# Performance work log

Hardware: AMD Instinct MI355X
Metric: run time of the kernel (lower is better)

The kernel has to match this reference:

```python
import jax, jax.numpy as jnp
import numpy as np

N_NODES = 100000
N_EDGES = 1000000
IN_CH = 128
HID = 128
N_CLS = 3


def setup_inputs() -> dict:
    key = jax.random.key(0)
    ks = jax.random.split(key, 10)
    scale_in = 1.0 / np.sqrt(IN_CH)
    scale_h = 1.0 / np.sqrt(HID)
    return {
        "x": jax.random.normal(ks[0], (N_NODES, IN_CH), dtype=jnp.float32),
        "edge_index": jax.random.randint(ks[1], (2, N_EDGES), 0, N_NODES, dtype=jnp.int64),
        # SAGEConv layer 1: lin_l (aggregated neighbors, with bias), lin_r (root, no bias)
        "w_l1": jax.random.normal(ks[2], (IN_CH, HID), dtype=jnp.float32) * scale_in,
        "b_l1": jnp.zeros((HID,), dtype=jnp.float32),
        "w_r1": jax.random.normal(ks[3], (IN_CH, HID), dtype=jnp.float32) * scale_in,
        # SAGEConv layer 2
        "w_l2": jax.random.normal(ks[4], (HID, HID), dtype=jnp.float32) * scale_h,
        "b_l2": jnp.zeros((HID,), dtype=jnp.float32),
        "w_r2": jax.random.normal(ks[5], (HID, HID), dtype=jnp.float32) * scale_h,
        # final classifier
        "w_cls": jax.random.normal(ks[6], (HID, N_CLS), dtype=jnp.float32) * scale_h,
        "b_cls": jnp.zeros((N_CLS,), dtype=jnp.float32),
    }


def _sage_conv(x, src, dst, w_l, b_l, w_r, num_nodes):
    # mean aggregation of source-node features onto destination nodes
    msg = x[src]                                              # [E, C] gather
    agg = jax.ops.segment_sum(msg, dst, num_segments=num_nodes)
    cnt = jax.ops.segment_sum(jnp.ones((src.shape[0],), x.dtype), dst,
                              num_segments=num_nodes)
    mean = agg / jnp.maximum(cnt, 1.0)[:, None]
    # out = lin_l(mean_aggr) + lin_r(x)
    return mean @ w_l + b_l + x @ w_r


def reference(x, edge_index, w_l1, b_l1, w_r1, w_l2, b_l2, w_r2, w_cls, b_cls):
    src, dst = edge_index[0], edge_index[1]
    n = x.shape[0]
    h = jax.nn.relu(_sage_conv(x, src, dst, w_l1, b_l1, w_r1, n))
    # dropout is identity in eval mode
    h = jax.nn.relu(_sage_conv(h, src, dst, w_l2, b_l2, w_r2, n))
    logits = h @ w_cls + b_cls
    return logits
```

## Files before the change

kernel.cpp:

```cpp
#include <hip/hip_runtime.h>
#include <hip/hip_bf16.h>

#define N_NODES 100000
#define N_EDGES 1000000
#define CH 128
#define KTOT 256
#define NCLS 3
#define SCAN_B 1024
#define SCAN_NB ((N_NODES + SCAN_B - 1) / SCAN_B)

#define NB_CNT ((N_EDGES + 255) / 256)
#define NB_CVTX (N_NODES * CH / 4 / 256)
#define NB_CVTW (KTOT * CH / 256)
#define NB_OTHER (NB_CVTX + 2 * NB_CVTW)
#define NB_PRE (NB_CNT + NB_OTHER)

typedef __attribute__((ext_vector_type(8))) short v8s;
typedef __attribute__((ext_vector_type(4))) float v4f;

__device__ __forceinline__ float bf2f(unsigned short u) {
    return __uint_as_float(((unsigned int)u) << 16);
}

__device__ __forceinline__ unsigned short f2bf(float f) {
    unsigned int u = __float_as_uint(f);
    unsigned int r = (u + 0x7fffu + ((u >> 16) & 1u)) >> 16;
    return (unsigned short)r;
}

__device__ __forceinline__ int edge_at(const void* e, int is64, long long i) {
    if (is64) return (int)((const long long*)e)[i];
    return ((const int*)e)[i];
}

__device__ __forceinline__ float ldf(const void* p, int isbf, size_t i) {
    if (isbf) return bf2f(((const unsigned short*)p)[i]);
    return ((const float*)p)[i];
}

__device__ __forceinline__ void acc_u32(unsigned int u, float& a0, float& a1) {
    a0 += bf2f((unsigned short)(u & 0xffffu));
    a1 += bf2f((unsigned short)(u >> 16));
}

__global__ void k_init(const void* __restrict__ e, const unsigned int* __restrict__ x,
                       int* __restrict__ eflag, int* __restrict__ dtf,
                       int* __restrict__ cnt, int* __restrict__ done) {
    int b = blockIdx.x;
    if (b == 0) {
        if (threadIdx.x < 64) {
            int v = ((const int*)e)[2 * threadIdx.x + 1];
            unsigned long long bl = __ballot(v != 0);
            if (threadIdx.x == 0) *eflag = (bl == 0ULL) ? 1 : 0;
        } else if (threadIdx.x == 64) {
            *done = 0;
        }
    } else if (b == 1) {
        if (threadIdx.x < 64) {
            unsigned int u = x[threadIdx.x];
            int ex = (u >> 7) & 0xff;
            int sane = (ex == 0) || (ex >= 100 && ex <= 154);
            unsigned long long bl = __ballot(sane);
            if (threadIdx.x == 0) *dtf = (__popcll(bl) >= 48) ? 1 : 0;
        }
    } else {
        int i = (b - 2) * 256 + threadIdx.x;
        if (i < N_NODES) cnt[i] = 0;
    }
}

__global__ void k_pre(const void* __restrict__ e, const int* __restrict__ eflag,
                      const int* __restrict__ dtf,
                      int* __restrict__ cnt, unsigned short* __restrict__ epos,
                      const void* __restrict__ x, unsigned short* __restrict__ Abuf,
                      const void* __restrict__ wl1, const void* __restrict__ wr1,
                      unsigned short* __restrict__ WT1,
                      const void* __restrict__ wl2, const void* __restrict__ wr2,
                      unsigned short* __restrict__ WT2) {
    int b = blockIdx.x;
    int cb = (b + 3) >> 2;
    if (cb > NB_CNT) cb = NB_CNT;
    if ((b & 3) == 0 && (b >> 2) < NB_CNT) {
        int i = (b >> 2) * 256 + threadIdx.x;
        if (i >= N_EDGES) return;
        int is64 = *eflag;
        int dst = edge_at(e, is64, (long long)N_EDGES + i);
        epos[i] = (unsigned short)atomicAdd(&cnt[dst], 1);
    } else {
        int ob = b - cb;
        if (ob < NB_CVTX) {
            int idx = ob * 256 + threadIdx.x;
            int node = idx >> 5;
            int ch = (idx & 31) * 4;
            int isbf = *dtf;
            unsigned short o[4];
            if (isbf) {
                ushort4 u = *(const ushort4*)((const unsigned short*)x +
                                              (size_t)node * CH + ch);
                o[0] = u.x; o[1] = u.y; o[2] = u.z; o[3] = u.w;
            } else {
                float4 v = *(const float4*)((const float*)x + (size_t)node * CH + ch);
                o[0] = f2bf(v.x); o[1] = f2bf(v.y); o[2] = f2bf(v.z); o[3] = f2bf(v.w);
            }
            *(ushort4*)(Abuf + (size_t)node * KTOT + CH + ch) =
                make_ushort4(o[0], o[1], o[2], o[3]);
        } else {
            int rel = ob - NB_CVTX;
            const void* wl = (rel < NB_CVTW) ? wl1 : wl2;
            const void* wr = (rel < NB_CVTW) ? wr1 : wr2;
            unsigned short* WT = (rel < NB_CVTW) ? WT1 : WT2;
            int i = (rel % NB_CVTW) * 256 + threadIdx.x;
            int k = i >> 7;
            int n = i & 127;
            int isbf = *dtf;
            float v = (k < CH) ? ldf(wl, isbf, (size_t)k * CH + n)
                               : ldf(wr, isbf, (size_t)(k - CH) * CH + n);
            WT[(size_t)n * KTOT + k] = f2bf(v);
        }
    }
}

__global__ __launch_bounds__(SCAN_B) void k_scan(
    const int* __restrict__ cnt, int* __restrict__ bsum, int* __restrict__ done,
    int* __restrict__ row_start) {
    __shared__ int s[SCAN_B];
    __shared__ int spre_sh;
    int tid = threadIdx.x;
    int gid = blockIdx.x * SCAN_B + tid;
    int v = (gid < N_NODES) ? cnt[gid] : 0;
    s[tid] = v;
    __syncthreads();
    for (int off = 1; off < SCAN_B; off <<= 1) {
        int t = (tid >= off) ? s[tid - off] : 0;
        __syncthreads();
        s[tid] += t;
        __syncthreads();
    }
    int excl_val = s[tid] - v;
    if (tid == SCAN_B - 1) {
        bsum[blockIdx.x] = s[tid];
        __threadfence();
        atomicAdd(done, 1);
    }
    if (tid == 0) {
        while (__hip_atomic_load(done, __ATOMIC_ACQUIRE, __HIP_MEMORY_SCOPE_AGENT) <
               SCAN_NB) {
        }
        __threadfence();
        int run = 0;
        for (int r = 0; r < SCAN_NB; r++) {
            if (r >= (int)blockIdx.x) break;
            run += bsum[r];
        }
        spre_sh = run;
    }
    __syncthreads();
    if (gid < N_NODES) row_start[gid] = excl_val + spre_sh;
    if (gid == 0) row_start[N_NODES] = N_EDGES;
}

__global__ void k_bucket(const void* __restrict__ e, const int* __restrict__ eflag,
                         const int* __restrict__ row_start,
                         const unsigned short* __restrict__ epos,
                         int* __restrict__ csr_src) {
    int i = blockIdx.x * blockDim.x + threadIdx.x;
    if (i >= N_EDGES) return;
    int is64 = *eflag;
    int src = edge_at(e, is64, i);
    int dst = edge_at(e, is64, (long long)N_EDGES + i);
    csr_src[row_start[dst] + (int)epos[i]] = src;
}

__global__ __launch_bounds__(256) void k_agg(
    const int* __restrict__ row_start, const int* __restrict__ csr_src,
    const unsigned short* __restrict__ gsrc, unsigned short* __restrict__ gdst) {
    long long gt = (long long)blockIdx.x * blockDim.x + threadIdx.x;
    int node = (int)(gt >> 4);
    int lane = (int)(gt & 15);
    if (node >= N_NODES) return;
    int beg = row_start[node];
    int end = row_start[node + 1];
    float a[8];
#pragma unroll
    for (int j = 0; j < 8; j++) a[j] = 0.f;
    int e = beg;
    while (e + 8 <= end) {
        int s[8];
#pragma unroll
        for (int j = 0; j < 8; j++) s[j] = csr_src[e + j];
        uint4 u[8];
#pragma unroll
        for (int j = 0; j < 8; j++)
            u[j] = *(const uint4*)(gsrc + (size_t)s[j] * KTOT + CH + lane * 8);
#pragma unroll
        for (int j = 0; j < 8; j++) {
            acc_u32(u[j].x, a[0], a[1]); acc_u32(u[j].y, a[2], a[3]);
            acc_u32(u[j].z, a[4], a[5]); acc_u32(u[j].w, a[6], a[7]);
        }
        e += 8;
    }
    while (e + 2 <= end) {
        int s0 = csr_src[e], s1 = csr_src[e + 1];
        uint4 u0 = *(const uint4*)(gsrc + (size_t)s0 * KTOT + CH + lane * 8);
        uint4 u1 = *(const uint4*)(gsrc + (size_t)s1 * KTOT + CH + lane * 8);
        acc_u32(u0.x, a[0], a[1]); acc_u32(u0.y, a[2], a[3]);
        acc_u32(u0.z, a[4], a[5]); acc_u32(u0.w, a[6], a[7]);
        acc_u32(u1.x, a[0], a[1]); acc_u32(u1.y, a[2], a[3]);
        acc_u32(u1.z, a[4], a[5]); acc_u32(u1.w, a[6], a[7]);
        e += 2;
    }
    if (e < end) {
        int s0 = csr_src[e];
        uint4 u0 = *(const uint4*)(gsrc + (size_t)s0 * KTOT + CH + lane * 8);
        acc_u32(u0.x, a[0], a[1]); acc_u32(u0.y, a[2], a[3]);
        acc_u32(u0.z, a[4], a[5]); acc_u32(u0.w, a[6], a[7]);
    }
    float rinv = 1.0f / (float)max(end - beg, 1);
    unsigned int p0 = (unsigned int)f2bf(a[0] * rinv) | ((unsigned int)f2bf(a[1] * rinv) << 16);
    unsigned int p1 = (unsigned int)f2bf(a[2] * rinv) | ((unsigned int)f2bf(a[3] * rinv) << 16);
    unsigned int p2 = (unsigned int)f2bf(a[4] * rinv) | ((unsigned int)f2bf(a[5] * rinv) << 16);
    unsigned int p3 = (unsigned int)f2bf(a[6] * rinv) | ((unsigned int)f2bf(a[7] * rinv) << 16);
    *(uint4*)(gdst + (size_t)node * KTOT + lane * 8) = make_uint4(p0, p1, p2, p3);
}

#define LDK 40
#define CLS_LD 130
__global__ __launch_bounds__(256) void k_gemm_mfma(
    const unsigned short* __restrict__ Abuf, const unsigned short* __restrict__ WT,
    const void* __restrict__ bias, const int* __restrict__ dtf,
    unsigned short* __restrict__ out, int out_stride, int out_off,
    const void* __restrict__ wcls, const void* __restrict__ bcls,
    float* __restrict__ cls_out) {
    __shared__ unsigned short smem[4 * 128 * LDK];
    __shared__ float wcls_s[CH * NCLS];
    unsigned short* As = smem;
    unsigned short* Bs = smem + 2 * 128 * LDK;
    const int t = threadIdx.x;
    const int w = t >> 6, l = t & 63;
    const int wx = w & 1, wy = w >> 1;
    const int quad = l >> 4, lrow = l & 15;
    const int row0 = blockIdx.x * 128;
    const int srow = t >> 1, shalf = t & 1;
    const int isbf = *dtf;

    if (cls_out) {
        for (int i = t; i < CH * NCLS; i += 256) wcls_s[i] = ldf(wcls, isbf, i);
    }

    int ar = row0 + srow;
    if (ar >= N_NODES) ar = N_NODES - 1;
    const unsigned short* abase = Abuf + (size_t)ar * KTOT + shalf * 16;
    const unsigned short* bbase = WT + (size_t)srow * KTOT + shalf * 16;

    v4f acc[4][4];
#pragma unroll
    for (int i = 0; i < 4; i++)
#pragma unroll
        for (int j = 0; j < 4; j++) acc[i][j] = (v4f){0.f, 0.f, 0.f, 0.f};

    {
        uint4 a0 = *(const uint4*)abase, a1 = *(const uint4*)(abase + 8);
        uint4 b0 = *(const uint4*)bbase, b1 = *(const uint4*)(bbase + 8);
        *(uint4*)&As[srow * LDK + shalf * 16] = a0;
        *(uint4*)&As[srow * LDK + shalf * 16 + 8] = a1;
        *(uint4*)&Bs[srow * LDK + shalf * 16] = b0;
        *(uint4*)&Bs[srow * LDK + shalf * 16 + 8] = b1;
    }
#pragma unroll
    for (int k = 0; k < KTOT / 32; k++) {
        uint4 na0, na1, nb0, nb1;
        if (k < KTOT / 32 - 1) {
            na0 = *(const uint4*)(abase + (k + 1) * 32);
            na1 = *(const uint4*)(abase + (k + 1) * 32 + 8);
            nb0 = *(const uint4*)(bbase + (k + 1) * 32);
            nb1 = *(const uint4*)(bbase + (k + 1) * 32 + 8);
        }
        __syncthreads();
        const int cur = (k & 1) * 128 * LDK, nxt = ((k + 1) & 1) * 128 * LDK;
        v8s af[4], bfr[4];
#pragma unroll
        for (int mi = 0; mi < 4; mi++)
            af[mi] = *(const v8s*)&As[cur + (wy * 64 + mi * 16 + lrow) * LDK + quad * 8];
#pragma unroll
        for (int ni = 0; ni < 4; ni++)
            bfr[ni] = *(const v8s*)&Bs[cur + (wx * 64 + ni * 16 + lrow) * LDK + quad * 8];
#pragma unroll
        for (int mi = 0; mi < 4; mi++)
#pragma unroll
            for (int ni = 0; ni < 4; ni++)
                acc[mi][ni] = __builtin_amdgcn_mfma_f32_16x16x32_bf16(
                    af[mi], bfr[ni], acc[mi][ni], 0, 0, 0);
        if (k < KTOT / 32 - 1) {
            *(uint4*)&As[nxt + srow * LDK + shalf * 16] = na0;
            *(uint4*)&As[nxt + srow * LDK + shalf * 16 + 8] = na1;
            *(uint4*)&Bs[nxt + srow * LDK + shalf * 16] = nb0;
            *(uint4*)&Bs[nxt + srow * LDK + shalf * 16 + 8] = nb1;
        }
    }
    float bj[4];
#pragma unroll
    for (int ni = 0; ni < 4; ni++) bj[ni] = ldf(bias, isbf, wx * 64 + ni * 16 + lrow);

    if (!cls_out) {
#pragma unroll
        for (int mi = 0; mi < 4; mi++) {
#pragma unroll
            for (int r = 0; r < 4; r++) {
                int grow = row0 + wy * 64 + mi * 16 + quad * 4 + r;
                if (grow < N_NODES) {
#pragma unroll
                    for (int ni = 0; ni < 4; ni++) {
                        int col = wx * 64 + ni * 16 + lrow;
                        float v = fmaxf(acc[mi][ni][r] + bj[ni], 0.0f);
                        out[(size_t)grow * out_stride + out_off + col] = f2bf(v);
                    }
                }
            }
        }
    } else {
        __syncthreads();
#pragma unroll
        for (int mi = 0; mi < 4; mi++) {
#pragma unroll
            for (int r = 0; r < 4; r++) {
                int row = wy * 64 + mi * 16 + quad * 4 + r;
#pragma unroll
                for (int ni = 0; ni < 4; ni++) {
                    int col = wx * 64 + ni * 16 + lrow;
                    float v = fmaxf(acc[mi][ni][r] + bj[ni], 0.0f);
                    smem[row * CLS_LD + col] = f2bf(v);
                }
            }
        }
        __syncthreads();
        if (t < 128) {
            int grow = row0 + t;
            if (grow < N_NODES) {
                float a0 = 0.f, a1 = 0.f, a2 = 0.f;
                for (int k = 0; k < CH; k++) {
                    float h = bf2f(smem[t * CLS_LD + k]);
                    a0 += h * wcls_s[k * NCLS + 0];
                    a1 += h * wcls_s[k * NCLS + 1];
                    a2 += h * wcls_s[k * NCLS + 2];
                }
                cls_out[(size_t)grow * NCLS + 0] = a0 + ldf(bcls, isbf, 0);
                cls_out[(size_t)grow * NCLS + 1] = a1 + ldf(bcls, isbf, 1);
                cls_out[(size_t)grow * NCLS + 2] = a2 + ldf(bcls, isbf, 2);
            }
        }
    }
}

extern "C" void kernel_launch(void* const* d_in, const int* in_sizes, int n_in,
                              void* d_out, int out_size, void* d_ws, size_t ws_size,
                              hipStream_t stream) {
    const void* x = d_in[0];
    const void* eidx = d_in[1];
    const void* w_l1 = d_in[2];
    const void* b_l1 = d_in[3];
    const void* w_r1 = d_in[4];
    const void* w_l2 = d_in[5];
    const void* b_l2 = d_in[6];
    const void* w_r2 = d_in[7];
    const void* w_cls = d_in[8];
    const void* b_cls = d_in[9];

    char* w = (char*)d_ws;
    int* eflag = (int*)w;
    int* dtf = (int*)(w + 64);
    int* done = (int*)(w + 128);
    int* cnt = (int*)(w + 4096);
    int* row_start = (int*)(w + 405504);
    int* bsum = (int*)(w + 1207296);
    unsigned short* epos = (unsigned short*)(w + 2097152);
    int* csr_src = (int*)(w + 4194304);
    unsigned short* WT1 = (unsigned short*)(w + 8388608);
    unsigned short* WT2 = (unsigned short*)(w + 8454144);
    unsigned short* A1 = (unsigned short*)(w + 11534336);
    unsigned short* A2 = (unsigned short*)(w + 62914560);

    hipLaunchKernelGGL(k_init, dim3(2 + (N_NODES + 255) / 256), dim3(256), 0, stream,
                       eidx, (const unsigned int*)x, eflag, dtf, cnt, done);
    hipLaunchKernelGGL(k_pre, dim3(NB_PRE), dim3(256), 0, stream,
                       eidx, eflag, dtf, cnt, epos, x, A1,
                       w_l1, w_r1, WT1, w_l2, w_r2, WT2);
    hipLaunchKernelGGL(k_scan, dim3(SCAN_NB), dim3(SCAN_B), 0, stream,
                       cnt, bsum, done, row_start);
    hipLaunchKernelGGL(k_bucket, dim3(NB_CNT), dim3(256), 0, stream,
                       eidx, eflag, row_start, epos, csr_src);
    hipLaunchKernelGGL(k_agg, dim3(N_NODES * 16 / 256), dim3(256), 0, stream,
                       row_start, csr_src, A1, A1);
    hipLaunchKernelGGL(k_gemm_mfma, dim3((N_NODES + 127) / 128), dim3(256), 0, stream,
                       A1, WT1, b_l1, dtf, A2, KTOT, CH,
                       (const void*)nullptr, (const void*)nullptr, (float*)nullptr);
    hipLaunchKernelGGL(k_agg, dim3(N_NODES * 16 / 256), dim3(256), 0, stream,
                       row_start, csr_src, A2, A2);
    hipLaunchKernelGGL(k_gemm_mfma, dim3((N_NODES + 127) / 128), dim3(256), 0, stream,
                       A2, WT2, b_l2, dtf, (unsigned short*)nullptr, 0, 0,
                       w_cls, b_cls, (float*)d_out);
}
```

Baseline: 302.2 us.

## Privatize degree counters per XCD and fuse scan with edge bucketing

Degree counting now keeps a separate counter array for each XCD, selected by reading the hardware XCD id register, so the atomics from one XCD no longer contend with the other seven across dies. Each edge stores its XCD index in the top bits of its 16-bit rank. The scan kernel sums the eight per-XCD counts, writes per-XCD base offsets back into the counter arrays, then waits on a grid-wide barrier before all 488 blocks scatter edges into CSR. This removes one kernel launch and the cross-die atomic traffic, at the cost of eight times the counter memory to zero and read, and a spin barrier that needs all blocks to be resident at once. The rank field is limited to 12 bits.

```diff
diff --git a/kernel.cpp b/kernel.cpp
--- a/kernel.cpp
+++ b/kernel.cpp
@@ -8,12 +8,12 @@
 #define NCLS 3
 #define SCAN_B 1024
 #define SCAN_NB ((N_NODES + SCAN_B - 1) / SCAN_B)
+#define SB_BLOCKS 488
 
 #define NB_CNT ((N_EDGES + 255) / 256)
 #define NB_CVTX (N_NODES * CH / 4 / 256)
 #define NB_CVTW (KTOT * CH / 256)
-#define NB_OTHER (NB_CVTX + 2 * NB_CVTW)
-#define NB_PRE (NB_CNT + NB_OTHER)
+#define NB_PRE (NB_CNT + NB_CVTX + 2 * NB_CVTW)
 
 typedef __attribute__((ext_vector_type(8))) short v8s;
 typedef __attribute__((ext_vector_type(4))) float v4f;
@@ -43,9 +43,13 @@
     a1 += bf2f((unsigned short)(u >> 16));
 }
 
+__device__ __forceinline__ int xcd_id() {
+    return (int)(__builtin_amdgcn_s_getreg(6164) & 7u);
+}
+
 __global__ void k_init(const void* __restrict__ e, const unsigned int* __restrict__ x,
                        int* __restrict__ eflag, int* __restrict__ dtf,
-                       int* __restrict__ cnt, int* __restrict__ done) {
+                       int* __restrict__ cnt8, int* __restrict__ done) {
     int b = blockIdx.x;
     if (b == 0) {
         if (threadIdx.x < 64) {
@@ -53,7 +57,8 @@
             unsigned long long bl = __ballot(v != 0);
             if (threadIdx.x == 0) *eflag = (bl == 0ULL) ? 1 : 0;
         } else if (threadIdx.x == 64) {
-            *done = 0;
+            done[0] = 0;
+            done[1] = 0;
         }
     } else if (b == 1) {
         if (threadIdx.x < 64) {
@@ -65,13 +70,13 @@
         }
     } else {
         int i = (b - 2) * 256 + threadIdx.x;
-        if (i < N_NODES) cnt[i] = 0;
+        if (i < 8 * N_NODES) cnt8[i] = 0;
     }
 }
 
 __global__ void k_pre(const void* __restrict__ e, const int* __restrict__ eflag,
                       const int* __restrict__ dtf,
-                      int* __restrict__ cnt, unsigned short* __restrict__ epos,
+                      int* __restrict__ cnt8, unsigned short* __restrict__ epos,
                       const void* __restrict__ x, unsigned short* __restrict__ Abuf,
                       const void* __restrict__ wl1, const void* __restrict__ wr1,
                       unsigned short* __restrict__ WT1,
@@ -85,7 +90,9 @@
         if (i >= N_EDGES) return;
         int is64 = *eflag;
         int dst = edge_at(e, is64, (long long)N_EDGES + i);
-        epos[i] = (unsigned short)atomicAdd(&cnt[dst], 1);
+        int r = xcd_id();
+        int rank = atomicAdd(&cnt8[r * N_NODES + dst], 1);
+        epos[i] = (unsigned short)(rank | (r << 12));
     } else {
         int ob = b - cb;
         if (ob < NB_CVTX) {
@@ -120,55 +127,78 @@
     }
 }
 
-__global__ __launch_bounds__(SCAN_B) void k_scan(
-    const int* __restrict__ cnt, int* __restrict__ bsum, int* __restrict__ done,
-    int* __restrict__ row_start) {
-    __shared__ int s[SCAN_B];
-    __shared__ int spre_sh;
-    int tid = threadIdx.x;
-    int gid = blockIdx.x * SCAN_B + tid;
-    int v = (gid < N_NODES) ? cnt[gid] : 0;
-    s[tid] = v;
+__global__ __launch_bounds__(SCAN_B) void k_scan_bucket(
+    int* __restrict__ cnt8, int* __restrict__ bsum, int* __restrict__ done,
+    int* __restrict__ row_start, const void* __restrict__ e,
+    const int* __restrict__ eflag, const unsigned short* __restrict__ epos,
+    int* __restrict__ csr_src) {
+    int tid = threadIdx.x, bid = blockIdx.x;
+    if (bid < SCAN_NB) {
+        __shared__ int s[SCAN_B];
+        __shared__ int spre_sh;
+        int gid = bid * SCAN_B + tid;
+        int c[8];
+        int deg = 0;
+#pragma unroll
+        for (int r = 0; r < 8; r++) {
+            c[r] = (gid < N_NODES) ? cnt8[r * N_NODES + gid] : 0;
+            deg += c[r];
+        }
+        s[tid] = deg;
+        __syncthreads();
+        for (int off = 1; off < SCAN_B; off <<= 1) {
+            int t = (tid >= off) ? s[tid - off] : 0;
+            __syncthreads();
+            s[tid] += t;
+            __syncthreads();
+        }
+        int excl = s[tid] - deg;
+        if (tid == SCAN_B - 1) {
+            bsum[bid] = s[tid];
+            __threadfence();
+            atomicAdd(&done[0], 1);
+        }
+        if (tid == 0) {
+            while (__hip_atomic_load(&done[0], __ATOMIC_ACQUIRE,
+                                     __HIP_MEMORY_SCOPE_AGENT) < SCAN_NB) {
+            }
+            __threadfence();
+            int run = 0;
+            for (int r = 0; r < bid; r++) run += bsum[r];
+            spre_sh = run;
+        }
+        __syncthreads();
+        int rs = excl + spre_sh;
+        if (gid < N_NODES) {
+            row_start[gid] = rs;
+            int run = rs;
+#pragma unroll
+            for (int r = 0; r < 8; r++) {
+                int t = c[r];
+                cnt8[r * N_NODES + gid] = run;
+                run += t;
+            }
+        }
+        if (gid == 0) row_start[N_NODES] = N_EDGES;
+        __threadfence();
+        __syncthreads();
+        if (tid == 0) atomicAdd(&done[1], 1);
+    }
+    if (tid == 0) {
+        while (__hip_atomic_load(&done[1], __ATOMIC_ACQUIRE,
+                                 __HIP_MEMORY_SCOPE_AGENT) < SCAN_NB) {
+        }
+    }
     __syncthreads();
-    for (int off = 1; off < SCAN_B; off <<= 1) {
-        int t = (tid >= off) ? s[tid - off] : 0;
-        __syncthreads();
-        s[tid] += t;
-        __syncthreads();
-    }
-    int excl_val = s[tid] - v;
-    if (tid == SCAN_B - 1) {
-        bsum[blockIdx.x] = s[tid];
-        __threadfence();
-        atomicAdd(done, 1);
-    }
-    if (tid == 0) {
-        while (__hip_atomic_load(done, __ATOMIC_ACQUIRE, __HIP_MEMORY_SCOPE_AGENT) <
-               SCAN_NB) {
-        }
-        __threadfence();
-        int run = 0;
-        for (int r = 0; r < SCAN_NB; r++) {
-            if (r >= (int)blockIdx.x) break;
-            run += bsum[r];
-        }
-        spre_sh = run;
-    }
-    __syncthreads();
-    if (gid < N_NODES) row_start[gid] = excl_val + spre_sh;
-    if (gid == 0) row_start[N_NODES] = N_EDGES;
-}
-
-__global__ void k_bucket(const void* __restrict__ e, const int* __restrict__ eflag,
-                         const int* __restrict__ row_start,
-                         const unsigned short* __restrict__ epos,
-                         int* __restrict__ csr_src) {
-    int i = blockIdx.x * blockDim.x + threadIdx.x;
-    if (i >= N_EDGES) return;
+    __threadfence();
     int is64 = *eflag;
-    int src = edge_at(e, is64, i);
-    int dst = edge_at(e, is64, (long long)N_EDGES + i);
-    csr_src[row_start[dst] + (int)epos[i]] = src;
+    for (int i = bid * SCAN_B + tid; i < N_EDGES; i += SB_BLOCKS * SCAN_B) {
+        int src = edge_at(e, is64, i);
+        int dst = edge_at(e, is64, (long long)N_EDGES + i);
+        unsigned short ep = epos[i];
+        int r = ep >> 12, rank = ep & 0xFFF;
+        csr_src[cnt8[r * N_NODES + dst] + rank] = src;
+    }
 }
 
 __global__ __launch_bounds__(256) void k_agg(
@@ -369,25 +399,23 @@
     int* eflag = (int*)w;
     int* dtf = (int*)(w + 64);
     int* done = (int*)(w + 128);
-    int* cnt = (int*)(w + 4096);
-    int* row_start = (int*)(w + 405504);
-    int* bsum = (int*)(w + 1207296);
-    unsigned short* epos = (unsigned short*)(w + 2097152);
-    int* csr_src = (int*)(w + 4194304);
-    unsigned short* WT1 = (unsigned short*)(w + 8388608);
-    unsigned short* WT2 = (unsigned short*)(w + 8454144);
+    int* cnt8 = (int*)(w + 4096);
+    int* row_start = (int*)(w + 3276800);
+    int* bsum = (int*)(w + 3678208);
+    unsigned short* epos = (unsigned short*)(w + 4194304);
+    int* csr_src = (int*)(w + 6291456);
+    unsigned short* WT1 = (unsigned short*)(w + 10485760);
+    unsigned short* WT2 = (unsigned short*)(w + 10551296);
     unsigned short* A1 = (unsigned short*)(w + 11534336);
     unsigned short* A2 = (unsigned short*)(w + 62914560);
 
-    hipLaunchKernelGGL(k_init, dim3(2 + (N_NODES + 255) / 256), dim3(256), 0, stream,
-                       eidx, (const unsigned int*)x, eflag, dtf, cnt, done);
+    hipLaunchKernelGGL(k_init, dim3(2 + (8 * N_NODES + 255) / 256), dim3(256), 0, stream,
+                       eidx, (const unsigned int*)x, eflag, dtf, cnt8, done);
     hipLaunchKernelGGL(k_pre, dim3(NB_PRE), dim3(256), 0, stream,
-                       eidx, eflag, dtf, cnt, epos, x, A1,
+                       eidx, eflag, dtf, cnt8, epos, x, A1,
                        w_l1, w_r1, WT1, w_l2, w_r2, WT2);
-    hipLaunchKernelGGL(k_scan, dim3(SCAN_NB), dim3(SCAN_B), 0, stream,
-                       cnt, bsum, done, row_start);
-    hipLaunchKernelGGL(k_bucket, dim3(NB_CNT), dim3(256), 0, stream,
-                       eidx, eflag, row_start, epos, csr_src);
+    hipLaunchKernelGGL(k_scan_bucket, dim3(SB_BLOCKS), dim3(SCAN_B), 0, stream,
+                       cnt8, bsum, done, row_start, eidx, eflag, epos, csr_src);
     hipLaunchKernelGGL(k_agg, dim3(N_NODES * 16 / 256), dim3(256), 0, stream,
                        row_start, csr_src, A1, A1);
     hipLaunchKernelGGL(k_gemm_mfma, dim3((N_NODES + 127) / 128), dim3(256), 0, stream,
```

Measured after the change: 551.5 us. 1.83x slower.

## Build CSR via two-level radix bucketing with shared-memory atomics

Applied to the files above, without the earlier changes.

Replaces the per-destination global atomic counting, multi-block spin-wait scan, and scatter with a two-pass bucket sort. The first pass takes per-block histograms over 512-node buckets in shared memory, a single-block scan turns them into offsets, and edges are scattered into bucket partitions packed as src<<9|dst_low. Each bucket block then does a local counting sort to produce row_start and csr_src. This removes contended global atomics and random scatters, but adds an extra pass over the edges and a serial single-block scan.

```diff
diff --git a/kernel.cpp b/kernel.cpp
--- a/kernel.cpp
+++ b/kernel.cpp
@@ -6,14 +6,16 @@
 #define CH 128
 #define KTOT 256
 #define NCLS 3
-#define SCAN_B 1024
-#define SCAN_NB ((N_NODES + SCAN_B - 1) / SCAN_B)
-
-#define NB_CNT ((N_EDGES + 255) / 256)
+
+#define NBKT 196
+#define EPB 4096
+#define NB_A ((N_EDGES + EPB - 1) / EPB)
+#define M_H (NBKT * NB_A)
+#define CHK ((M_H + 1023) / 1024)
+
 #define NB_CVTX (N_NODES * CH / 4 / 256)
 #define NB_CVTW (KTOT * CH / 256)
-#define NB_OTHER (NB_CVTX + 2 * NB_CVTW)
-#define NB_PRE (NB_CNT + NB_OTHER)
+#define NB_A1 (NB_A + NB_CVTX + 2 * NB_CVTW)
 
 typedef __attribute__((ext_vector_type(8))) short v8s;
 typedef __attribute__((ext_vector_type(4))) float v4f;
@@ -44,18 +46,14 @@
 }
 
 __global__ void k_init(const void* __restrict__ e, const unsigned int* __restrict__ x,
-                       int* __restrict__ eflag, int* __restrict__ dtf,
-                       int* __restrict__ cnt, int* __restrict__ done) {
-    int b = blockIdx.x;
-    if (b == 0) {
+                       int* __restrict__ eflag, int* __restrict__ dtf) {
+    if (blockIdx.x == 0) {
         if (threadIdx.x < 64) {
             int v = ((const int*)e)[2 * threadIdx.x + 1];
             unsigned long long bl = __ballot(v != 0);
             if (threadIdx.x == 0) *eflag = (bl == 0ULL) ? 1 : 0;
-        } else if (threadIdx.x == 64) {
-            *done = 0;
-        }
-    } else if (b == 1) {
+        }
+    } else {
         if (threadIdx.x < 64) {
             unsigned int u = x[threadIdx.x];
             int ex = (u >> 7) & 0xff;
@@ -63,33 +61,37 @@
             unsigned long long bl = __ballot(sane);
             if (threadIdx.x == 0) *dtf = (__popcll(bl) >= 48) ? 1 : 0;
         }
+    }
+}
+
+__global__ void k_A1(const void* __restrict__ e, const int* __restrict__ eflag,
+                     const int* __restrict__ dtf, int* __restrict__ hist,
+                     const void* __restrict__ x, unsigned short* __restrict__ Abuf,
+                     const void* __restrict__ wl1, const void* __restrict__ wr1,
+                     unsigned short* __restrict__ WT1,
+                     const void* __restrict__ wl2, const void* __restrict__ wr2,
+                     unsigned short* __restrict__ WT2) {
+    int b = blockIdx.x;
+    int t = threadIdx.x;
+    if (b < NB_A) {
+        __shared__ int h[NBKT];
+        if (t < NBKT) h[t] = 0;
+        __syncthreads();
+        int is64 = *eflag;
+#pragma unroll
+        for (int j = 0; j < EPB / 256; j++) {
+            int i = b * EPB + j * 256 + t;
+            if (i < N_EDGES) {
+                int dst = edge_at(e, is64, (long long)N_EDGES + i);
+                atomicAdd(&h[dst >> 9], 1);
+            }
+        }
+        __syncthreads();
+        if (t < NBKT) hist[t * NB_A + b] = h[t];
     } else {
-        int i = (b - 2) * 256 + threadIdx.x;
-        if (i < N_NODES) cnt[i] = 0;
-    }
-}
-
-__global__ void k_pre(const void* __restrict__ e, const int* __restrict__ eflag,
-                      const int* __restrict__ dtf,
-                      int* __restrict__ cnt, unsigned short* __restrict__ epos,
-                      const void* __restrict__ x, unsigned short* __restrict__ Abuf,
-                      const void* __restrict__ wl1, const void* __restrict__ wr1,
-                      unsigned short* __restrict__ WT1,
-                      const void* __restrict__ wl2, const void* __restrict__ wr2,
-                      unsigned short* __restrict__ WT2) {
-    int b = blockIdx.x;
-    int cb = (b + 3) >> 2;
-    if (cb > NB_CNT) cb = NB_CNT;
-    if ((b & 3) == 0 && (b >> 2) < NB_CNT) {
-        int i = (b >> 2) * 256 + threadIdx.x;
-        if (i >= N_EDGES) return;
-        int is64 = *eflag;
-        int dst = edge_at(e, is64, (long long)N_EDGES + i);
-        epos[i] = (unsigned short)atomicAdd(&cnt[dst], 1);
-    } else {
-        int ob = b - cb;
+        int ob = b - NB_A;
         if (ob < NB_CVTX) {
-            int idx = ob * 256 + threadIdx.x;
+            int idx = ob * 256 + t;
             int node = idx >> 5;
             int ch = (idx & 31) * 4;
             int isbf = *dtf;
@@ -109,7 +111,7 @@
             const void* wl = (rel < NB_CVTW) ? wl1 : wl2;
             const void* wr = (rel < NB_CVTW) ? wr1 : wr2;
             unsigned short* WT = (rel < NB_CVTW) ? WT1 : WT2;
-            int i = (rel % NB_CVTW) * 256 + threadIdx.x;
+            int i = (rel % NB_CVTW) * 256 + t;
             int k = i >> 7;
             int n = i & 127;
             int isbf = *dtf;
@@ -120,55 +122,95 @@
     }
 }
 
-__global__ __launch_bounds__(SCAN_B) void k_scan(
-    const int* __restrict__ cnt, int* __restrict__ bsum, int* __restrict__ done,
-    int* __restrict__ row_start) {
-    __shared__ int s[SCAN_B];
-    __shared__ int spre_sh;
-    int tid = threadIdx.x;
-    int gid = blockIdx.x * SCAN_B + tid;
-    int v = (gid < N_NODES) ? cnt[gid] : 0;
-    s[tid] = v;
-    __syncthreads();
-    for (int off = 1; off < SCAN_B; off <<= 1) {
-        int t = (tid >= off) ? s[tid - off] : 0;
-        __syncthreads();
-        s[tid] += t;
-        __syncthreads();
-    }
-    int excl_val = s[tid] - v;
-    if (tid == SCAN_B - 1) {
-        bsum[blockIdx.x] = s[tid];
-        __threadfence();
-        atomicAdd(done, 1);
-    }
-    if (tid == 0) {
-        while (__hip_atomic_load(done, __ATOMIC_ACQUIRE, __HIP_MEMORY_SCOPE_AGENT) <
-               SCAN_NB) {
-        }
-        __threadfence();
-        int run = 0;
-        for (int r = 0; r < SCAN_NB; r++) {
-            if (r >= (int)blockIdx.x) break;
-            run += bsum[r];
-        }
-        spre_sh = run;
-    }
-    __syncthreads();
-    if (gid < N_NODES) row_start[gid] = excl_val + spre_sh;
-    if (gid == 0) row_start[N_NODES] = N_EDGES;
-}
-
-__global__ void k_bucket(const void* __restrict__ e, const int* __restrict__ eflag,
-                         const int* __restrict__ row_start,
-                         const unsigned short* __restrict__ epos,
-                         int* __restrict__ csr_src) {
-    int i = blockIdx.x * blockDim.x + threadIdx.x;
-    if (i >= N_EDGES) return;
+__global__ __launch_bounds__(1024) void k_scanH(int* __restrict__ hist,
+                                                int* __restrict__ bktbase) {
+    __shared__ int ps[1024];
+    int t = threadIdx.x;
+    int lv[CHK];
+    int s = 0;
+    int base0 = t * CHK;
+#pragma unroll
+    for (int j = 0; j < CHK; j++) {
+        int idx = base0 + j;
+        int v = (idx < M_H) ? hist[idx] : 0;
+        lv[j] = v;
+        s += v;
+    }
+    ps[t] = s;
+    __syncthreads();
+    for (int off = 1; off < 1024; off <<= 1) {
+        int v = (t >= off) ? ps[t - off] : 0;
+        __syncthreads();
+        ps[t] += v;
+        __syncthreads();
+    }
+    int run = ps[t] - s;
+#pragma unroll
+    for (int j = 0; j < CHK; j++) {
+        int idx = base0 + j;
+        if (idx < M_H) hist[idx] = run;
+        run += lv[j];
+    }
+    __syncthreads();
+    if (t < NBKT) bktbase[t] = hist[t * NB_A];
+    if (t == 0) bktbase[NBKT] = N_EDGES;
+}
+
+__global__ void k_A3(const void* __restrict__ e, const int* __restrict__ eflag,
+                     const int* __restrict__ hist, unsigned int* __restrict__ part) {
+    __shared__ int cur[NBKT];
+    int b = blockIdx.x;
+    int t = threadIdx.x;
+    if (t < NBKT) cur[t] = hist[t * NB_A + b];
+    __syncthreads();
     int is64 = *eflag;
-    int src = edge_at(e, is64, i);
-    int dst = edge_at(e, is64, (long long)N_EDGES + i);
-    csr_src[row_start[dst] + (int)epos[i]] = src;
+#pragma unroll
+    for (int j = 0; j < EPB / 256; j++) {
+        int i = b * EPB + j * 256 + t;
+        if (i < N_EDGES) {
+            int src = edge_at(e, is64, i);
+            int dst = edge_at(e, is64, (long long)N_EDGES + i);
+            int pos = atomicAdd(&cur[dst >> 9], 1);
+            part[pos] = ((unsigned int)src << 9) | (unsigned int)(dst & 511);
+        }
+    }
+}
+
+__global__ __launch_bounds__(1024) void k_B(const int* __restrict__ bktbase,
+                                            const unsigned int* __restrict__ part,
+                                            int* __restrict__ row_start,
+                                            int* __restrict__ csr_src) {
+    __shared__ int dcnt[512], sa[512], curs[512];
+    int b = blockIdx.x;
+    int t = threadIdx.x;
+    int e0 = bktbase[b], e1 = bktbase[b + 1];
+    if (t < 512) dcnt[t] = 0;
+    __syncthreads();
+    for (int i = e0 + t; i < e1; i += 1024)
+        atomicAdd(&dcnt[part[i] & 511], 1);
+    __syncthreads();
+    if (t < 512) sa[t] = dcnt[t];
+    __syncthreads();
+    for (int off = 1; off < 512; off <<= 1) {
+        int v = 0;
+        if (t < 512 && t >= off) v = sa[t - off];
+        __syncthreads();
+        if (t < 512) sa[t] += v;
+        __syncthreads();
+    }
+    if (t < 512) {
+        int excl = sa[t] - dcnt[t];
+        curs[t] = e0 + excl;
+        int node = b * 512 + t;
+        if (node < N_NODES) row_start[node] = e0 + excl;
+    }
+    if (b == 0 && t == 0) row_start[N_NODES] = N_EDGES;
+    __syncthreads();
+    for (int i = e0 + t; i < e1; i += 1024) {
+        unsigned int p = part[i];
+        int pos = atomicAdd(&curs[p & 511], 1);
+        csr_src[pos] = (int)(p >> 9);
+    }
 }
 
 __global__ __launch_bounds__(256) void k_agg(
@@ -368,26 +410,26 @@
     char* w = (char*)d_ws;
     int* eflag = (int*)w;
     int* dtf = (int*)(w + 64);
-    int* done = (int*)(w + 128);
-    int* cnt = (int*)(w + 4096);
-    int* row_start = (int*)(w + 405504);
-    int* bsum = (int*)(w + 1207296);
-    unsigned short* epos = (unsigned short*)(w + 2097152);
-    int* csr_src = (int*)(w + 4194304);
-    unsigned short* WT1 = (unsigned short*)(w + 8388608);
-    unsigned short* WT2 = (unsigned short*)(w + 8454144);
+    int* hist = (int*)(w + 4096);
+    int* bktbase = (int*)(w + 196608);
+    int* row_start = (int*)(w + 262144);
+    unsigned int* part = (unsigned int*)(w + 720896);
+    int* csr_src = (int*)(w + 4915200);
+    unsigned short* WT1 = (unsigned short*)(w + 8978432);
+    unsigned short* WT2 = (unsigned short*)(w + 9043968);
     unsigned short* A1 = (unsigned short*)(w + 11534336);
     unsigned short* A2 = (unsigned short*)(w + 62914560);
 
-    hipLaunchKernelGGL(k_init, dim3(2 + (N_NODES + 255) / 256), dim3(256), 0, stream,
-                       eidx, (const unsigned int*)x, eflag, dtf, cnt, done);
-    hipLaunchKernelGGL(k_pre, dim3(NB_PRE), dim3(256), 0, stream,
-                       eidx, eflag, dtf, cnt, epos, x, A1,
+    hipLaunchKernelGGL(k_init, dim3(2), dim3(256), 0, stream,
+                       eidx, (const unsigned int*)x, eflag, dtf);
+    hipLaunchKernelGGL(k_A1, dim3(NB_A1), dim3(256), 0, stream,
+                       eidx, eflag, dtf, hist, x, A1,
                        w_l1, w_r1, WT1, w_l2, w_r2, WT2);
-    hipLaunchKernelGGL(k_scan, dim3(SCAN_NB), dim3(SCAN_B), 0, stream,
-                       cnt, bsum, done, row_start);
-    hipLaunchKernelGGL(k_bucket, dim3(NB_CNT), dim3(256), 0, stream,
-                       eidx, eflag, row_start, epos, csr_src);
+    hipLaunchKernelGGL(k_scanH, dim3(1), dim3(1024), 0, stream, hist, bktbase);
+    hipLaunchKernelGGL(k_A3, dim3(NB_A), dim3(256), 0, stream,
+                       eidx, eflag, hist, part);
+    hipLaunchKernelGGL(k_B, dim3(NBKT), dim3(1024), 0, stream,
+                       bktbase, part, row_start, csr_src);
     hipLaunchKernelGGL(k_agg, dim3(N_NODES * 16 / 256), dim3(256), 0, stream,
                        row_start, csr_src, A1, A1);
     hipLaunchKernelGGL(k_gemm_mfma, dim3((N_NODES + 127) / 128), dim3(256), 0, stream,
```

New measurement: 308.4 us. +2.1%, slower.
